# Performance work log

Measured on AMD Instinct MI355X. Metric: run time of the kernel, lower is better.

## Reference

```python
import jax, jax.numpy as jnp
import numpy as np

B, L, W = 64, 20, 48
D = W * W           # 2304, MoE input/output size (image_width**2)
E = 4               # num_experts
HID = 2 * D         # expert hidden size
K = 1               # top_k
LOSS_COEF = 1e-2


def _cv_squared(x):
    # torch: x.var() (unbiased) / (x.mean()**2 + eps)
    eps = 1e-10
    return jnp.var(x, ddof=1) / (jnp.mean(x) ** 2 + eps)


def _moe(x, w_gate, w1, b1, w2, b2):
    # Noisy top-k gating, inference path (train=False => clean logits, no noise).
    logits = x @ w_gate                                   # [B, E]
    top_logits, top_idx = jax.lax.top_k(logits, K + 1)    # min(k+1, E)
    topk_gates = jax.nn.softmax(top_logits[:, :K], axis=-1)
    gates = jnp.zeros_like(logits).at[
        jnp.arange(x.shape[0])[:, None], top_idx[:, :K]
    ].set(topk_gates)                                     # [B, E] sparse gates
    importance = gates.sum(0)
    load = (gates > 0).sum(0).astype(x.dtype)             # _gates_to_load
    aux = LOSS_COEF * (_cv_squared(importance) + _cv_squared(load))
    # Dense expert compute weighted by gates (same math as dispatch/combine).
    h = jax.nn.relu(jnp.einsum('bd,edh->beh', x, w1) + b1)      # [B,E,HID]
    y = jnp.einsum('beh,ehd->bed', h, w2) + b2                  # [B,E,D]
    out = jnp.einsum('be,bed->bd', gates, y)                    # [B,D]
    return out, aux


def _conv3d(x, w, b, pad):
    y = jax.lax.conv_general_dilated(
        x, w, window_strides=(1, 1, 1), padding=pad,
        dimension_numbers=('NCDHW', 'OIDHW', 'NCDHW'))
    return y + b[None, :, None, None, None]


def _forward(input, conv1_w, conv1_b, conv2_w, conv2_b,
             t_gate, t_w1, t_b1, t_w2, t_b2,
             a_gate, a_w1, a_b1, a_w2, a_b2,
             q_gate, q_w1, q_b1, q_w2, q_b2,
             enc_w, enc_b, dec_w, dec_b):
    x = jnp.transpose(input, (0, 2, 1, 3, 4))                   # [B,1,L,H,W]
    x = jax.nn.relu(_conv3d(x, conv1_w, conv1_b, ((1, 1), (1, 1), (1, 1))))
    x = jax.nn.relu(_conv3d(x, conv2_w, conv2_b, ((0, 0), (1, 1), (1, 1))))  # [B,1,1,H,W]
    xf = x.reshape(x.shape[0], -1)                              # [B, D]
    transform, l1 = _moe(xf, t_gate, t_w1, t_b1, t_w2, t_b2)
    add, l2 = _moe(xf, a_gate, a_w1, a_b1, a_w2, a_b2)
    quad, l3 = _moe(xf, q_gate, q_w1, q_b1, q_w2, q_b2)
    s = input.shape                                             # [B,L,1,H,W]
    transform = transform.reshape(s[0], 1, s[2], s[3], s[4])
    add = add.reshape(s[0], 1, s[2], s[3], s[4])
    quad = quad.reshape(s[0], 1, s[2], s[3], s[4])
    out = input * input * quad + input * transform + add        # [B,L,1,H,W]
    # encoder = Linear(D,D)+ReLU, decoder = Linear(D,D) over flattened H*W
    of = out.reshape(s[0], s[1], D)
    of = jax.nn.relu(of @ enc_w + enc_b)
    of = of @ dec_w + dec_b
    of = jax.nn.sigmoid(of)
    return of.reshape(s), l1 + l2 + l3


def setup_inputs() -> dict:
    key = jax.random.key(0)
    ks = jax.random.split(key, 32)
    sc = 0.02
    inp = {
        'input': jax.random.normal(ks[0], (B, L, 1, W, W), jnp.float32),
        'conv1_w': jax.random.normal(ks[1], (10, 1, 3, 3, 3), jnp.float32) * sc,
        'conv1_b': jnp.zeros((10,), jnp.float32),
        'conv2_w': jax.random.normal(ks[2], (1, 10, L, 3, 3), jnp.float32) * sc,
        'conv2_b': jnp.zeros((1,), jnp.float32),
        'enc_w': jax.random.normal(ks[3], (D, D), jnp.float32) * sc,
        'enc_b': jnp.zeros((D,), jnp.float32),
        'dec_w': jax.random.normal(ks[4], (D, D), jnp.float32) * sc,
        'dec_b': jnp.zeros((D,), jnp.float32),
    }
    for i, p in enumerate(['t', 'a', 'q']):
        k0, k1, k2 = jax.random.split(ks[5 + i], 3)
        inp[p + '_gate'] = jnp.zeros((D, E), jnp.float32) + jax.random.normal(k0, (D, E), jnp.float32) * sc
        inp[p + '_w1'] = jax.random.normal(k1, (E, D, HID), jnp.float32) * sc
        inp[p + '_b1'] = jnp.zeros((E, HID), jnp.float32)
        inp[p + '_w2'] = jax.random.normal(k2, (E, HID, D), jnp.float32) * sc
        inp[p + '_b2'] = jnp.zeros((E, D), jnp.float32)
    return inp


def reference(input, conv1_w, conv1_b, conv2_w, conv2_b,
              t_gate, t_w1, t_b1, t_w2, t_b2,
              a_gate, a_w1, a_b1, a_w2, a_b2,
              q_gate, q_w1, q_b1, q_w2, q_b2,
              enc_w, enc_b, dec_w, dec_b):
    return _forward(input, conv1_w, conv1_b, conv2_w, conv2_b,
                    t_gate, t_w1, t_b1, t_w2, t_b2,
                    a_gate, a_w1, a_b1, a_w2, a_b2,
                    q_gate, q_w1, q_b1, q_w2, q_b2,
                    enc_w, enc_b, dec_w, dec_b)
```

## Files before the change

kernel.cpp:

```cpp
#include <hip/hip_runtime.h>
#include <stdint.h>

#define NB 64
#define NL 20
#define ND 2304
#define NE 4
#define NH 4608
#define NM 1280

typedef float f32x4 __attribute__((ext_vector_type(4)));
typedef __bf16 bf16x8 __attribute__((ext_vector_type(8)));
typedef unsigned short u16;
typedef u16 u16x4 __attribute__((ext_vector_type(4)));
typedef unsigned int u32;
typedef u32 u32x4 __attribute__((ext_vector_type(4)));

__device__ __forceinline__ u16 f2bf(float f) {
  u32 u = __builtin_bit_cast(u32, f);
  u += 0x7fffu + ((u >> 16) & 1u);
  return (u16)(u >> 16);
}

__device__ __forceinline__ void gl_lds16(const void* g, void* l) {
  __builtin_amdgcn_global_load_lds(
      (const __attribute__((address_space(1))) void*)g,
      (__attribute__((address_space(3))) void*)l, 16, 0, 0);
}

#define OFF_XFACC 0
#define OFF_XF    147456
#define OFF_H     294912
#define OFF_Y     1179648
#define OFF_AUX   1622016
#define OFF_CNT   1622020
#define OFF_ROWS  1622032
#define OFF_OFB   1622240
#define OFF_H1B   3096800
#define OFF_ENCWB 4571360
#define OFF_DECWB 7225568
#define OFF_XC    9879776
#define OFF_P     10322144

__global__ __launch_bounds__(256) void k_conv(
    const float* __restrict__ in, const float* __restrict__ w1,
    const float* __restrict__ b1, const float* __restrict__ w2,
    float* __restrict__ xfp) {
  __shared__ float insl[3][50][50];
  __shared__ float c1[2][50][50];
  __shared__ float w1s[270];
  __shared__ float w2s[90];
  __shared__ float b1s[10];
  const int d = blockIdx.x, b = blockIdx.y, t = threadIdx.x;
  for (int i = t; i < 270; i += 256) w1s[i] = w1[i];
  for (int i = t; i < 90; i += 256) w2s[i] = w2[(size_t)((i / 9) * 20 + d) * 9 + (i % 9)];
  if (t < 10) b1s[t] = b1[t];
  for (int i = t; i < 7500; i += 256) {
    int s = i / 2500, rr = (i % 2500) / 50, cc = i % 50;
    int gd = d - 1 + s, gy = rr - 1, gx = cc - 1;
    float v = 0.f;
    if (gd >= 0 && gd < NL && (unsigned)gy < 48u && (unsigned)gx < 48u)
      v = in[((size_t)b * NL + gd) * ND + gy * 48 + gx];
    insl[s][rr][cc] = v;
  }
  for (int i = t; i < 5000; i += 256) ((float*)c1)[i] = 0.f;
  float s2[3][4];
#pragma unroll
  for (int qi = 0; qi < 3; ++qi)
#pragma unroll
    for (int xq = 0; xq < 4; ++xq) s2[qi][xq] = 0.f;
  __syncthreads();
  for (int pc = 0; pc < 5; ++pc) {
#pragma unroll
    for (int qi = 0; qi < 3; ++qi) {
      int q = t + qi * 256;
      if (q < 576) {
        int y = q / 12, x0 = (q % 12) * 4;
        float a0[4], a1[4];
        const float bb0 = b1s[2 * pc], bb1 = b1s[2 * pc + 1];
#pragma unroll
        for (int xq = 0; xq < 4; ++xq) { a0[xq] = bb0; a1[xq] = bb1; }
#pragma unroll
        for (int kd = 0; kd < 3; ++kd)
#pragma unroll
          for (int ky = 0; ky < 3; ++ky) {
            float v[6];
#pragma unroll
            for (int i = 0; i < 6; ++i) v[i] = insl[kd][y + ky][x0 + i];
            const float* wa = &w1s[(2 * pc) * 27 + kd * 9 + ky * 3];
            const float* wb = wa + 27;
#pragma unroll
            for (int xq = 0; xq < 4; ++xq) {
              a0[xq] += v[xq] * wa[0] + v[xq + 1] * wa[1] + v[xq + 2] * wa[2];
              a1[xq] += v[xq] * wb[0] + v[xq + 1] * wb[1] + v[xq + 2] * wb[2];
            }
          }
#pragma unroll
        for (int xq = 0; xq < 4; ++xq) {
          c1[0][y + 1][x0 + 1 + xq] = fmaxf(a0[xq], 0.f);
          c1[1][y + 1][x0 + 1 + xq] = fmaxf(a1[xq], 0.f);
        }
      }
    }
    __syncthreads();
#pragma unroll
    for (int qi = 0; qi < 3; ++qi) {
      int q = t + qi * 256;
      if (q < 576) {
        int y = q / 12, x0 = (q % 12) * 4;
#pragma unroll
        for (int cc = 0; cc < 2; ++cc) {
#pragma unroll
          for (int ky = 0; ky < 3; ++ky) {
            float v[6];
#pragma unroll
            for (int i = 0; i < 6; ++i) v[i] = c1[cc][y + ky][x0 + i];
            const float* wr = &w2s[(2 * pc + cc) * 9 + ky * 3];
#pragma unroll
            for (int xq = 0; xq < 4; ++xq)
              s2[qi][xq] += v[xq] * wr[0] + v[xq + 1] * wr[1] + v[xq + 2] * wr[2];
          }
        }
      }
    }
    __syncthreads();
  }
#pragma unroll
  for (int qi = 0; qi < 3; ++qi) {
    int q = t + qi * 256;
    if (q < 576) {
      f32x4 o = {s2[qi][0], s2[qi][1], s2[qi][2], s2[qi][3]};
      *(f32x4*)(xfp + ((size_t)d * NB + b) * ND + q * 4) = o;
    }
  }
}

__global__ __launch_bounds__(256) void k_bias_relu(
    const float* __restrict__ xfp, const float* __restrict__ c2b, float* __restrict__ xf) {
  const size_t i = (size_t)blockIdx.x * 256 + threadIdx.x;
  float s = c2b[0];
#pragma unroll
  for (int d = 0; d < NL; ++d) s += xfp[(size_t)d * (NB * ND) + i];
  xf[i] = fmaxf(s, 0.f);
}

__global__ __launch_bounds__(256) void k_gate(
    const float* __restrict__ xf,
    const float* __restrict__ g0, const float* __restrict__ g1, const float* __restrict__ g2,
    float* __restrict__ aux, int* __restrict__ cnt, int* __restrict__ rows) {
  const int p = blockIdx.x, t = threadIdx.x;
  const float* __restrict__ g = (p == 0) ? g0 : ((p == 1) ? g1 : g2);
  __shared__ float lg[64][4];
  __shared__ int lidx[64];
  __shared__ int lcnt[4];
  if (t < 4) lcnt[t] = 0;
  const int wv = t >> 6, l = t & 63;
  for (int b0 = 0; b0 < 64; b0 += 4) {
    int bb = b0 + wv;
    f32x4 acc = {0.f, 0.f, 0.f, 0.f};
    const float* xr = xf + (size_t)bb * ND + l * 36;
    const float* gr = g + (size_t)l * 36 * 4;
#pragma unroll
    for (int i4 = 0; i4 < 9; ++i4) {
      f32x4 xv = *(const f32x4*)(xr + i4 * 4);
#pragma unroll
      for (int qq = 0; qq < 4; ++qq) {
        f32x4 gv = *(const f32x4*)(gr + (i4 * 4 + qq) * 4);
        acc += xv[qq] * gv;
      }
    }
#pragma unroll
    for (int e = 0; e < 4; ++e) {
      float pv = acc[e];
#pragma unroll
      for (int off = 32; off > 0; off >>= 1) pv += __shfl_down(pv, off);
      if (l == 0) lg[bb][e] = pv;
    }
  }
  __syncthreads();
  if (t < 64) {
    float best = lg[t][0];
    int bi = 0;
#pragma unroll
    for (int e = 1; e < 4; ++e)
      if (lg[t][e] > best) { best = lg[t][e]; bi = e; }
    lidx[t] = bi;
    atomicAdd(&lcnt[bi], 1);
  }
  __syncthreads();
  if (t == 0) {
    int ofs[4]; int run = 0;
#pragma unroll
    for (int e = 0; e < 4; ++e) { ofs[e] = run; run += lcnt[e]; cnt[p * 4 + e] = lcnt[e]; }
    for (int b = 0; b < 64; ++b) { int e = lidx[b]; rows[p * 64 + ofs[e]++] = b; }
    float var = 0.f;
#pragma unroll
    for (int e = 0; e < 4; ++e) { float dd = (float)lcnt[e] - 16.f; var += dd * dd; }
    var *= (1.f / 3.f);
    aux[p] = 0.02f * var / (256.f + 1e-10f);
  }
}

__global__ __launch_bounds__(256) void k_gather(
    const float* __restrict__ xf, const int* __restrict__ rows, u16* __restrict__ Xb) {
  const int slot = blockIdx.x, t = threadIdx.x;
  const int r = rows[slot];
  const f32x4* src = (const f32x4*)(xf + (size_t)r * ND);
  u16x4* dst = (u16x4*)(Xb + (size_t)slot * ND);
  for (int i = t; i < ND / 4; i += 256) {
    f32x4 v = src[i];
    u16x4 o;
#pragma unroll
    for (int q = 0; q < 4; ++q) o[q] = f2bf(v[q]);
    dst[i] = o;
  }
}

template <int K, int N, int KS>
__global__ __launch_bounds__(256) void k_moe_mfma(
    const u16* __restrict__ Xb,
    const float* __restrict__ wt, const float* __restrict__ wa, const float* __restrict__ wq,
    const int* __restrict__ cnt, float* __restrict__ P) {
  constexpr int KL = K / KS;
  constexpr int NT = KL / 32;
  const int tile = blockIdx.x;
  const int ks = blockIdx.y;
  const int pe = blockIdx.z >> 1, ch = blockIdx.z & 1;
  const int p = pe >> 2, e = pe & 3;
  const int c = cnt[p * 4 + e];
  const int rstart = ch * 32;
  if (rstart >= c) return;
  const int nrows = min(32, c - rstart);
  int pref = 0;
  for (int e2 = 0; e2 < e; ++e2) pref += cnt[p * 4 + e2];
  const int slot0 = p * 64 + pref + rstart;
  const float* __restrict__ W = (p == 0) ? wt : ((p == 1) ? wa : wq);
  __shared__ float wb[NT][8 * 260];
  const int t = threadIdx.x;
  const int w = t >> 6, l = t & 63;
  const int l15 = l & 15, l4 = l >> 4;
  const int mbase = (w & 1) * 16;
  const int nb0 = (w >> 1) * 32;

  int ar = slot0 + mbase + l15; if (ar > 191) ar = 191;
  const u16* Ag = Xb + (size_t)ar * K + ks * KL + l4 * 8;
  bf16x8 areg[NT];
#pragma unroll
  for (int kt = 0; kt < NT; ++kt) areg[kt] = *(const bf16x8*)(Ag + kt * 32);

  const float* Wg = W + (size_t)e * K * N + (size_t)(ks * KL) * N + tile * 64;
#pragma unroll
  for (int kt = 0; kt < NT; ++kt) {
#pragma unroll
    for (int j = 0; j < 2; ++j)
      gl_lds16(Wg + ((size_t)(kt * 32 + w * 8 + j * 4 + l4)) * N + l15 * 4,
               &wb[kt][(w * 2 + j) * 260]);
  }

  f32x4 acc[2] = {};

#define MOESTEP(KT, VM)                                                       \
  {                                                                           \
    asm volatile("s_waitcnt vmcnt(" #VM ")" ::: "memory");                    \
    __syncthreads();                                                          \
    const float* ww = &wb[KT][0];                                             \
    _Pragma("unroll")                                                         \
    for (int i = 0; i < 2; ++i) {                                             \
      const int nb = nb0 + i * 16 + l15;                                      \
      bf16x8 bfr;                                                             \
      _Pragma("unroll")                                                       \
      for (int jj = 0; jj < 8; ++jj)                                          \
        bfr[jj] = (__bf16)ww[(l4 * 2 + (jj >> 2)) * 260 + (jj & 3) * 64 + nb];\
      acc[i] = __builtin_amdgcn_mfma_f32_16x16x32_bf16(areg[KT], bfr, acc[i], 0, 0, 0); \
    }                                                                         \
  }

  MOESTEP(0, 16); MOESTEP(1, 14); MOESTEP(2, 12); MOESTEP(3, 10);
  MOESTEP(4, 8);  MOESTEP(5, 6);  MOESTEP(6, 4);  MOESTEP(7, 2);
  MOESTEP(8, 0);
#undef MOESTEP

  const size_t pbase = (size_t)ks * 192 * N;
#pragma unroll
  for (int i = 0; i < 2; ++i) {
    const int n = tile * 64 + nb0 + i * 16 + l15;
#pragma unroll
    for (int r = 0; r < 4; ++r) {
      const int m = mbase + l4 * 4 + r;
      if (m < nrows) P[pbase + (size_t)(slot0 + m) * N + n] = acc[i][r];
    }
  }
}

__global__ __launch_bounds__(256) void k_red1(
    const float* __restrict__ P,
    const float* __restrict__ b1t, const float* __restrict__ b1a, const float* __restrict__ b1q,
    const int* __restrict__ cnt, u16* __restrict__ Hb) {
  const int slot = blockIdx.y;
  const int p = slot >> 6, pos = slot & 63;
  int e = 0, run = cnt[p * 4];
  while (pos >= run && e < 3) { ++e; run += cnt[p * 4 + e]; }
  const float* __restrict__ b1 = (p == 0) ? b1t : ((p == 1) ? b1a : b1q);
  const int j0 = blockIdx.x * 1024 + threadIdx.x * 4;
  if (j0 >= NH) return;
  f32x4 s = *(const f32x4*)(b1 + (size_t)e * NH + j0);
#pragma unroll
  for (int ks = 0; ks < 8; ++ks)
    s += *(const f32x4*)(P + ((size_t)ks * 192 + slot) * NH + j0);
  u16x4 o;
#pragma unroll
  for (int q = 0; q < 4; ++q) o[q] = f2bf(fmaxf(s[q], 0.f));
  *(u16x4*)(Hb + (size_t)slot * NH + j0) = o;
}

__global__ __launch_bounds__(256) void k_red2(
    const float* __restrict__ P,
    const float* __restrict__ b2t, const float* __restrict__ b2a, const float* __restrict__ b2q,
    const int* __restrict__ cnt, const int* __restrict__ rows, float* __restrict__ Y) {
  const int slot = blockIdx.y;
  const int p = slot >> 6, pos = slot & 63;
  int e = 0, run = cnt[p * 4];
  while (pos >= run && e < 3) { ++e; run += cnt[p * 4 + e]; }
  const float* __restrict__ b2 = (p == 0) ? b2t : ((p == 1) ? b2a : b2q);
  const int b = rows[slot];
  const int t = threadIdx.x;
  if (t >= 192) return;
  const int j0 = blockIdx.x * 768 + t * 4;
  f32x4 s = *(const f32x4*)(b2 + (size_t)e * ND + j0);
#pragma unroll
  for (int ks = 0; ks < 16; ++ks)
    s += *(const f32x4*)(P + ((size_t)ks * 192 + slot) * ND + j0);
  *(f32x4*)(Y + (size_t)(p * 64 + b) * ND + j0) = s;
}

__global__ __launch_bounds__(256) void k_combine(
    const float* __restrict__ in, const float* __restrict__ Y, u16* __restrict__ ofb) {
  const size_t i = (size_t)blockIdx.x * 256 + threadIdx.x;
  const size_t e0 = i * 4;
  const int row = (int)(e0 / ND);
  const int d = (int)(e0 - (size_t)row * ND);
  const int b = row / NL;
  f32x4 v = *(const f32x4*)(in + e0);
  const size_t yb = (size_t)b * ND + d;
  f32x4 tt = *(const f32x4*)(Y + yb);
  f32x4 aa = *(const f32x4*)(Y + (size_t)64 * ND + yb);
  f32x4 qq = *(const f32x4*)(Y + (size_t)128 * ND + yb);
  u16x4 o;
#pragma unroll
  for (int q = 0; q < 4; ++q) {
    float f = v[q] * v[q] * qq[q] + v[q] * tt[q] + aa[q];
    o[q] = f2bf(f);
  }
  *(u16x4*)(ofb + e0) = o;
}

__global__ __launch_bounds__(256) void k_wt(
    const float* __restrict__ encw, const float* __restrict__ decw,
    u16* __restrict__ encb, u16* __restrict__ decb) {
  __shared__ float tl[32][33];
  const float* __restrict__ src = blockIdx.z ? decw : encw;
  u16* __restrict__ dst = blockIdx.z ? decb : encb;
  const int k0 = blockIdx.x * 32, n0 = blockIdx.y * 32;
  const int tx = threadIdx.x & 31, ty = threadIdx.x >> 5;
  for (int r = ty; r < 32; r += 8) tl[r][tx] = src[(size_t)(k0 + r) * ND + n0 + tx];
  __syncthreads();
  for (int r = ty; r < 32; r += 8) dst[(size_t)(n0 + r) * ND + k0 + tx] = f2bf(tl[tx][r]);
}

template <int MODE>
__global__ __launch_bounds__(256) void k_gemm(
    const u16* __restrict__ A, const u16* __restrict__ Bt,
    const float* __restrict__ bias, void* __restrict__ outp,
    const float* __restrict__ aux) {
  __shared__ u16 As[64 * 32];
  __shared__ u16 Bs[128 * 32];
  const int t = threadIdx.x;
  const int bm = blockIdx.x, bn = blockIdx.y;
  const int lane = t & 63;
  const int wr = (t >> 7) & 1, wc = (t >> 6) & 1;
  const int l15 = lane & 15, l4 = lane >> 4;
  f32x4 acc[2][4] = {};
  const int r0 = t >> 2, kc0 = (t & 3) * 8;
  const int r1 = (t + 256) >> 2, kc1 = ((t + 256) & 3) * 8;
  const size_t baseA = (size_t)(bm * 64) * ND;
  const size_t baseB = (size_t)(bn * 128) * ND;
  for (int k0 = 0; k0 < ND; k0 += 32) {
    *(u32x4*)(As + t * 8) = *(const u32x4*)(A + baseA + (size_t)r0 * ND + k0 + kc0);
    *(u32x4*)(Bs + t * 8) = *(const u32x4*)(Bt + baseB + (size_t)r0 * ND + k0 + kc0);
    *(u32x4*)(Bs + (t + 256) * 8) = *(const u32x4*)(Bt + baseB + (size_t)r1 * ND + k0 + kc1);
    __syncthreads();
    bf16x8 af[2], bfr[4];
#pragma unroll
    for (int i = 0; i < 2; ++i)
      af[i] = *(const bf16x8*)(As + (wr * 32 + i * 16 + l15) * 32 + l4 * 8);
#pragma unroll
    for (int i = 0; i < 4; ++i)
      bfr[i] = *(const bf16x8*)(Bs + (wc * 64 + i * 16 + l15) * 32 + l4 * 8);
#pragma unroll
    for (int mi = 0; mi < 2; ++mi)
#pragma unroll
      for (int ni = 0; ni < 4; ++ni)
        acc[mi][ni] = __builtin_amdgcn_mfma_f32_16x16x32_bf16(af[mi], bfr[ni], acc[mi][ni], 0, 0, 0);
    __syncthreads();
  }
  const int colbase = bn * 128 + wc * 64;
  const int rowbase = bm * 64 + wr * 32;
#pragma unroll
  for (int mi = 0; mi < 2; ++mi) {
#pragma unroll
    for (int ni = 0; ni < 4; ++ni) {
      const int colg = colbase + ni * 16 + l15;
      const float bv = bias[colg];
#pragma unroll
      for (int r = 0; r < 4; ++r) {
        const int rowg = rowbase + mi * 16 + l4 * 4 + r;
        float v = acc[mi][ni][r] + bv;
        if (MODE == 0) {
          ((u16*)outp)[(size_t)rowg * ND + colg] = f2bf(fmaxf(v, 0.f));
        } else {
          ((float*)outp)[(size_t)rowg * ND + colg] = 1.f / (1.f + __expf(-v));
        }
      }
    }
  }
  if (MODE == 1 && bm == 0 && bn == 0 && t == 0)
    ((float*)outp)[(size_t)NM * ND] = aux[0] + aux[1] + aux[2];
}

extern "C" void kernel_launch(void* const* d_in, const int* in_sizes, int n_in,
                              void* d_out, int out_size, void* d_ws, size_t ws_size,
                              hipStream_t stream) {
  (void)in_sizes; (void)n_in; (void)out_size; (void)ws_size;
  const float* input   = (const float*)d_in[0];
  const float* conv1_w = (const float*)d_in[1];
  const float* conv1_b = (const float*)d_in[2];
  const float* conv2_w = (const float*)d_in[3];
  const float* conv2_b = (const float*)d_in[4];
  const float* enc_w   = (const float*)d_in[5];
  const float* enc_b   = (const float*)d_in[6];
  const float* dec_w   = (const float*)d_in[7];
  const float* dec_b   = (const float*)d_in[8];
  const float* gate_t = (const float*)d_in[9];
  const float* w1_t   = (const float*)d_in[10];
  const float* b1_t   = (const float*)d_in[11];
  const float* w2_t   = (const float*)d_in[12];
  const float* b2_t   = (const float*)d_in[13];
  const float* gate_a = (const float*)d_in[14];
  const float* w1_a   = (const float*)d_in[15];
  const float* b1_a   = (const float*)d_in[16];
  const float* w2_a   = (const float*)d_in[17];
  const float* b2_a   = (const float*)d_in[18];
  const float* gate_q = (const float*)d_in[19];
  const float* w1_q   = (const float*)d_in[20];
  const float* b1_q   = (const float*)d_in[21];
  const float* w2_q   = (const float*)d_in[22];
  const float* b2_q   = (const float*)d_in[23];

  float* ws = (float*)d_ws;
  float* xf     = ws + OFF_XF;
  u16*   Hb     = (u16*)(ws + OFF_H);
  float* Y      = ws + OFF_Y;
  float* aux    = ws + OFF_AUX;
  int*   cnt    = (int*)(ws + OFF_CNT);
  int*   rows   = (int*)(ws + OFF_ROWS);
  u16*   ofb    = (u16*)(ws + OFF_OFB);
  u16*   h1b    = (u16*)(ws + OFF_H1B);
  u16*   encwb  = (u16*)(ws + OFF_ENCWB);
  u16*   decwb  = (u16*)(ws + OFF_DECWB);
  u16*   Xcb    = (u16*)(ws + OFF_XC);
  float* P      = ws + OFF_P;

  k_conv<<<dim3(20, 64), 256, 0, stream>>>(input, conv1_w, conv1_b, conv2_w, P);
  k_bias_relu<<<576, 256, 0, stream>>>(P, conv2_b, xf);
  k_wt<<<dim3(72, 72, 2), 256, 0, stream>>>(enc_w, dec_w, encwb, decwb);
  k_gate<<<3, 256, 0, stream>>>(xf, gate_t, gate_a, gate_q, aux, cnt, rows);
  k_gather<<<192, 256, 0, stream>>>(xf, rows, Xcb);
  k_moe_mfma<ND, NH, 8><<<dim3(72, 8, 24), 256, 0, stream>>>(Xcb, w1_t, w1_a, w1_q, cnt, P);
  k_red1<<<dim3(5, 192), 256, 0, stream>>>(P, b1_t, b1_a, b1_q, cnt, Hb);
  k_moe_mfma<NH, ND, 16><<<dim3(36, 16, 24), 256, 0, stream>>>(Hb, w2_t, w2_a, w2_q, cnt, P);
  k_red2<<<dim3(3, 192), 256, 0, stream>>>(P, b2_t, b2_a, b2_q, cnt, rows, Y);
  k_combine<<<2880, 256, 0, stream>>>(input, Y, ofb);
  k_gemm<0><<<dim3(20, 18), 256, 0, stream>>>(ofb, encwb, enc_b, (void*)h1b, aux);
  k_gemm<1><<<dim3(20, 18), 256, 0, stream>>>(h1b, decwb, dec_b, d_out, aux);
}
```

Before: 506.5 us.

## Split conv kernel spatially into three row bands with halo recompute

The fused conv1+conv2 kernel now splits each (depth, batch) slice into three 16-row bands via a third grid dimension. Each block loads a 20-row input halo and recomputes an 18-row conv1 band, so one thread handles one 4-wide output strip instead of up to three. This triples the block count and shrinks LDS per block, which should improve occupancy and load balance. The cost is redundant conv1 work on the halo rows and idle threads in each phase.

```diff
diff --git a/kernel.cpp b/kernel.cpp
--- a/kernel.cpp
+++ b/kernel.cpp
@@ -27,7 +27,6 @@
       (__attribute__((address_space(3))) void*)l, 16, 0, 0);
 }
 
-#define OFF_XFACC 0
 #define OFF_XF    147456
 #define OFF_H     294912
 #define OFF_Y     1179648
@@ -45,36 +44,32 @@
     const float* __restrict__ in, const float* __restrict__ w1,
     const float* __restrict__ b1, const float* __restrict__ w2,
     float* __restrict__ xfp) {
-  __shared__ float insl[3][50][50];
-  __shared__ float c1[2][50][50];
+  __shared__ float insl[3][20][50];
+  __shared__ float c1[2][18][50];
   __shared__ float w1s[270];
   __shared__ float w2s[90];
   __shared__ float b1s[10];
-  const int d = blockIdx.x, b = blockIdx.y, t = threadIdx.x;
+  const int d = blockIdx.x, b = blockIdx.y, h = blockIdx.z, t = threadIdx.x;
+  const int gy0 = h * 16;
   for (int i = t; i < 270; i += 256) w1s[i] = w1[i];
   for (int i = t; i < 90; i += 256) w2s[i] = w2[(size_t)((i / 9) * 20 + d) * 9 + (i % 9)];
   if (t < 10) b1s[t] = b1[t];
-  for (int i = t; i < 7500; i += 256) {
-    int s = i / 2500, rr = (i % 2500) / 50, cc = i % 50;
-    int gd = d - 1 + s, gy = rr - 1, gx = cc - 1;
+  for (int i = t; i < 3000; i += 256) {
+    int s = i / 1000, rr = (i % 1000) / 50, cc = i % 50;
+    int gd = d - 1 + s, gy = gy0 - 2 + rr, gx = cc - 1;
     float v = 0.f;
     if (gd >= 0 && gd < NL && (unsigned)gy < 48u && (unsigned)gx < 48u)
       v = in[((size_t)b * NL + gd) * ND + gy * 48 + gx];
     insl[s][rr][cc] = v;
   }
-  for (int i = t; i < 5000; i += 256) ((float*)c1)[i] = 0.f;
-  float s2[3][4];
-#pragma unroll
-  for (int qi = 0; qi < 3; ++qi)
-#pragma unroll
-    for (int xq = 0; xq < 4; ++xq) s2[qi][xq] = 0.f;
+  for (int i = t; i < 1800; i += 256) ((float*)c1)[i] = 0.f;
+  float s2[4] = {0.f, 0.f, 0.f, 0.f};
+  const int y1 = t / 12, x0 = (t % 12) * 4;
   __syncthreads();
   for (int pc = 0; pc < 5; ++pc) {
-#pragma unroll
-    for (int qi = 0; qi < 3; ++qi) {
-      int q = t + qi * 256;
-      if (q < 576) {
-        int y = q / 12, x0 = (q % 12) * 4;
+    if (t < 216) {
+      const int gr = gy0 - 1 + y1;
+      if ((unsigned)gr < 48u) {
         float a0[4], a1[4];
         const float bb0 = b1s[2 * pc], bb1 = b1s[2 * pc + 1];
 #pragma unroll
@@ -85,7 +80,7 @@
           for (int ky = 0; ky < 3; ++ky) {
             float v[6];
 #pragma unroll
-            for (int i = 0; i < 6; ++i) v[i] = insl[kd][y + ky][x0 + i];
+            for (int i = 0; i < 6; ++i) v[i] = insl[kd][y1 + ky][x0 + i];
             const float* wa = &w1s[(2 * pc) * 27 + kd * 9 + ky * 3];
             const float* wb = wa + 27;
 #pragma unroll
@@ -96,41 +91,32 @@
           }
 #pragma unroll
         for (int xq = 0; xq < 4; ++xq) {
-          c1[0][y + 1][x0 + 1 + xq] = fmaxf(a0[xq], 0.f);
-          c1[1][y + 1][x0 + 1 + xq] = fmaxf(a1[xq], 0.f);
+          c1[0][y1][x0 + 1 + xq] = fmaxf(a0[xq], 0.f);
+          c1[1][y1][x0 + 1 + xq] = fmaxf(a1[xq], 0.f);
         }
       }
     }
     __syncthreads();
-#pragma unroll
-    for (int qi = 0; qi < 3; ++qi) {
-      int q = t + qi * 256;
-      if (q < 576) {
-        int y = q / 12, x0 = (q % 12) * 4;
-#pragma unroll
-        for (int cc = 0; cc < 2; ++cc) {
-#pragma unroll
-          for (int ky = 0; ky < 3; ++ky) {
-            float v[6];
-#pragma unroll
-            for (int i = 0; i < 6; ++i) v[i] = c1[cc][y + ky][x0 + i];
-            const float* wr = &w2s[(2 * pc + cc) * 9 + ky * 3];
-#pragma unroll
-            for (int xq = 0; xq < 4; ++xq)
-              s2[qi][xq] += v[xq] * wr[0] + v[xq + 1] * wr[1] + v[xq + 2] * wr[2];
-          }
+    if (t < 192) {
+#pragma unroll
+      for (int cc = 0; cc < 2; ++cc) {
+#pragma unroll
+        for (int ky = 0; ky < 3; ++ky) {
+          float v[6];
+#pragma unroll
+          for (int i = 0; i < 6; ++i) v[i] = c1[cc][y1 + ky][x0 + i];
+          const float* wr = &w2s[(2 * pc + cc) * 9 + ky * 3];
+#pragma unroll
+          for (int xq = 0; xq < 4; ++xq)
+            s2[xq] += v[xq] * wr[0] + v[xq + 1] * wr[1] + v[xq + 2] * wr[2];
         }
       }
     }
     __syncthreads();
   }
-#pragma unroll
-  for (int qi = 0; qi < 3; ++qi) {
-    int q = t + qi * 256;
-    if (q < 576) {
-      f32x4 o = {s2[qi][0], s2[qi][1], s2[qi][2], s2[qi][3]};
-      *(f32x4*)(xfp + ((size_t)d * NB + b) * ND + q * 4) = o;
-    }
+  if (t < 192) {
+    f32x4 o = {s2[0], s2[1], s2[2], s2[3]};
+    *(f32x4*)(xfp + ((size_t)d * NB + b) * ND + (gy0 + y1) * 48 + x0) = o;
   }
 }
 
@@ -469,7 +455,7 @@
   u16*   Xcb    = (u16*)(ws + OFF_XC);
   float* P      = ws + OFF_P;
 
-  k_conv<<<dim3(20, 64), 256, 0, stream>>>(input, conv1_w, conv1_b, conv2_w, P);
+  k_conv<<<dim3(20, 64, 3), 256, 0, stream>>>(input, conv1_w, conv1_b, conv2_w, P);
   k_bias_relu<<<576, 256, 0, stream>>>(P, conv2_b, xf);
   k_wt<<<dim3(72, 72, 2), 256, 0, stream>>>(enc_w, dec_w, encwb, decwb);
   k_gate<<<3, 256, 0, stream>>>(xf, gate_t, gate_a, gate_q, aux, cnt, rows);
```

Result: faster. 494.1 us (-2.4%).
